# Optimization experiments

Hardware: AMD Instinct MI355X
Metric: run time of the kernel (lower is better)

The kernel has to match this reference:

```python
import jax, jax.numpy as jnp
import numpy as np

BETA = 0.1
MARGIN = 0.1
LOSS_WEIGHT = 1.0
K = 4          # num_negative_samples_per_positive
EPS = 1e-6
C, D, P = 100000, 256, 65536


def _energy(p, c):
    """Euclidean entailment-cone energy: relu(apex_angle(p,c) - aperture(p))."""
    diff = c - p
    num = jnp.sum(c * c, -1) - jnp.sum(p * p, -1) - jnp.sum(diff * diff, -1)
    norm_p = jnp.linalg.norm(p, axis=-1)
    denom = 2.0 * norm_p * jnp.linalg.norm(diff, axis=-1) + EPS
    cosang = jnp.clip(num / denom, -1.0 + EPS, 1.0 - EPS)
    ang = jnp.arccos(cosang)
    aperture = jnp.arcsin(jnp.clip(BETA / (norm_p + EPS), 0.0, 1.0 - EPS))
    return jax.nn.relu(ang - aperture)


def setup_inputs() -> dict:
    key = jax.random.key(0)
    k1, k2, k3 = jax.random.split(key, 3)
    prototypes = jax.random.normal(k1, (C, D), dtype=jnp.float32)
    pairs = jax.random.randint(k2, (P, 2), 0, C, dtype=jnp.int32)
    neg_c = jax.random.randint(k3, (P * K,), 0, C, dtype=jnp.int32)
    return {"prototypes": prototypes, "pairs": pairs, "neg_c": neg_c}


def reference(prototypes, pairs, neg_c):
    # positive pairs: (parent, child) gathers
    p_pos = prototypes[pairs[:, 0]]                    # [P, D]
    c_pos = prototypes[pairs[:, 1]]                    # [P, D]
    avg_pos = _energy(p_pos, c_pos).mean()

    # negatives: each positive parent repeated K times vs sampled neg children
    neg_p_idx = jnp.repeat(pairs[:, 0], K)             # [P*K]
    p_neg = prototypes[neg_p_idx]                      # [P*K, D]
    c_neg = prototypes[neg_c]                          # [P*K, D]
    avg_neg = jax.nn.relu(MARGIN - _energy(p_neg, c_neg)).mean()

    return (avg_pos + avg_neg) * 0.5 * LOSS_WEIGHT
```

## Files before the change

kernel.cpp:

```cpp
#include <hip/hip_runtime.h>

#define BETA   0.1f
#define MARGIN 0.1f
#define EPSF   1e-6f
#define KNEG   4

typedef float f2_t __attribute__((ext_vector_type(2)));

__device__ __forceinline__ float gsum16(float v) {
    #pragma unroll
    for (int off = 8; off >= 1; off >>= 1) v += __shfl_xor(v, off, 64);
    return v;
}
__device__ __forceinline__ float wave_sum(float v) {
    #pragma unroll
    for (int off = 32; off >= 1; off >>= 1) v += __shfl_xor(v, off, 64);
    return v;
}
__device__ __forceinline__ float dot4(float4 a, float4 b) {
    return a.x*b.x + a.y*b.y + a.z*b.z + a.w*b.w;
}
__device__ __forceinline__ void unpack4(unsigned int u, float* f) {
    f2_t a = __builtin_amdgcn_cvt_pk_f32_fp8(u, false);
    f[0] = a.x; f[1] = a.y;
    a = __builtin_amdgcn_cvt_pk_f32_fp8(u, true);
    f[2] = a.x; f[3] = a.y;
}

__global__ __launch_bounds__(256) void cvt_fp8(
    const float* __restrict__ in, unsigned int* __restrict__ out, int n4)
{
    int i = blockIdx.x * 256 + threadIdx.x;
    const int stride = gridDim.x * 256;
    const float4* in4 = (const float4*)in;
    for (; i < n4; i += stride) {
        float4 v = in4[i];
        unsigned int p = __builtin_amdgcn_cvt_pk_fp8_f32(v.x, v.y, 0u, false);
        p = __builtin_amdgcn_cvt_pk_fp8_f32(v.z, v.w, p, true);
        out[i] = p;
    }
}

__global__ __launch_bounds__(256) void cone_main_fp8(
    const uint4* __restrict__ tab,
    const int*   __restrict__ pairs,
    const int*   __restrict__ negc,
    float*       __restrict__ part,
    int P)
{
    const int lane = threadIdx.x & 63;
    const int wid  = threadIdx.x >> 6;
    const int sub  = lane >> 4;
    const int sl   = lane & 15;
    const int pair = (blockIdx.x * 4 + wid) * 4 + sub;

    float pos_e = 0.f, neg_e = 0.f;
    if (pair < P) {
        const int pi = pairs[2 * pair];
        int idx[5];
        idx[0] = pairs[2 * pair + 1];
        #pragma unroll
        for (int k = 0; k < KNEG; ++k) idx[1 + k] = negc[4 * pair + k];

        uint4 pu = tab[(size_t)pi * 16 + sl];
        uint4 cu[5];
        #pragma unroll
        for (int j = 0; j < 5; ++j) cu[j] = tab[(size_t)idx[j] * 16 + sl];

        float pf[16];
        unpack4(pu.x, pf + 0);  unpack4(pu.y, pf + 4);
        unpack4(pu.z, pf + 8);  unpack4(pu.w, pf + 12);
        float pp = 0.f;
        #pragma unroll
        for (int d = 0; d < 16; ++d) pp += pf[d] * pf[d];
        float p2     = gsum16(pp);
        float norm_p = sqrtf(p2);
        float apert  = asinf(fminf(fmaxf(BETA / (norm_p + EPSF), 0.f), 1.f - EPSF));

        #pragma unroll
        for (int j = 0; j < 5; ++j) {
            float cf[16];
            unpack4(cu[j].x, cf + 0);  unpack4(cu[j].y, cf + 4);
            unpack4(cu[j].z, cf + 8);  unpack4(cu[j].w, cf + 12);
            float cc = 0.f, dd = 0.f;
            #pragma unroll
            for (int d = 0; d < 16; ++d) {
                cc += cf[d] * cf[d];
                float t = cf[d] - pf[d];
                dd += t * t;
            }
            float c2 = gsum16(cc);
            float d2 = gsum16(dd);
            float num    = c2 - p2 - d2;
            float den    = 2.f * norm_p * sqrtf(d2) + EPSF;
            float cosang = fminf(fmaxf(num / den, -1.f + EPSF), 1.f - EPSF);
            float e      = fmaxf(acosf(cosang) - apert, 0.f);
            if (j == 0) pos_e = e;
            else        neg_e += fmaxf(MARGIN - e, 0.f);
        }
    }

    __shared__ float sp[16], sn[16];
    if (sl == 0) { sp[wid * 4 + sub] = pos_e; sn[wid * 4 + sub] = neg_e; }
    __syncthreads();
    if (threadIdx.x == 0) {
        float ps = 0.f, ns = 0.f;
        #pragma unroll
        for (int i = 0; i < 16; ++i) { ps += sp[i]; ns += sn[i]; }
        part[2 * blockIdx.x]     = ps;
        part[2 * blockIdx.x + 1] = ns;
    }
}

__global__ __launch_bounds__(256) void cone_main_f32(
    const float* __restrict__ proto,
    const int*   __restrict__ pairs,
    const int*   __restrict__ negc,
    float*       __restrict__ part,
    int P)
{
    const int lane = threadIdx.x & 63;
    const int wid  = threadIdx.x >> 6;
    const int sub  = lane >> 4;
    const int sl   = lane & 15;
    const int pair = (blockIdx.x * 4 + wid) * 4 + sub;

    float pos_e = 0.f, neg_e = 0.f;
    if (pair < P) {
        const int pi = pairs[2 * pair];
        int idx[5];
        idx[0] = pairs[2 * pair + 1];
        #pragma unroll
        for (int k = 0; k < KNEG; ++k) idx[1 + k] = negc[4 * pair + k];

        const float4* prow = (const float4*)(proto + (size_t)pi * 256);
        float4 pv[4];
        #pragma unroll
        for (int r = 0; r < 4; ++r) pv[r] = prow[sl + 16 * r];

        float pp = 0.f;
        #pragma unroll
        for (int r = 0; r < 4; ++r) pp += dot4(pv[r], pv[r]);
        float p2     = gsum16(pp);
        float norm_p = sqrtf(p2);
        float apert  = asinf(fminf(fmaxf(BETA / (norm_p + EPSF), 0.f), 1.f - EPSF));

        #pragma unroll
        for (int j = 0; j < 5; ++j) {
            const float4* crow = (const float4*)(proto + (size_t)idx[j] * 256);
            float cc = 0.f, dd = 0.f;
            #pragma unroll
            for (int r = 0; r < 4; ++r) {
                float4 c = crow[sl + 16 * r], p = pv[r];
                cc += dot4(c, c);
                float dx = c.x - p.x, dy = c.y - p.y, dz = c.z - p.z, dw = c.w - p.w;
                dd += dx*dx + dy*dy + dz*dz + dw*dw;
            }
            float c2 = gsum16(cc);
            float d2 = gsum16(dd);
            float num    = c2 - p2 - d2;
            float den    = 2.f * norm_p * sqrtf(d2) + EPSF;
            float cosang = fminf(fmaxf(num / den, -1.f + EPSF), 1.f - EPSF);
            float e      = fmaxf(acosf(cosang) - apert, 0.f);
            if (j == 0) pos_e = e;
            else        neg_e += fmaxf(MARGIN - e, 0.f);
        }
    }

    __shared__ float sp[16], sn[16];
    if (sl == 0) { sp[wid * 4 + sub] = pos_e; sn[wid * 4 + sub] = neg_e; }
    __syncthreads();
    if (threadIdx.x == 0) {
        float ps = 0.f, ns = 0.f;
        #pragma unroll
        for (int i = 0; i < 16; ++i) { ps += sp[i]; ns += sn[i]; }
        part[2 * blockIdx.x]     = ps;
        part[2 * blockIdx.x + 1] = ns;
    }
}

__global__ __launch_bounds__(1024) void cone_final(
    const float* __restrict__ part, float* __restrict__ out, int nblocks, int P)
{
    float ps = 0.f, ns = 0.f;
    for (int i = threadIdx.x; i < nblocks; i += 1024) {
        ps += part[2 * i];
        ns += part[2 * i + 1];
    }
    ps = wave_sum(ps);
    ns = wave_sum(ns);
    const int lane = threadIdx.x & 63, wid = threadIdx.x >> 6;
    __shared__ float sp[16], sn[16];
    if (lane == 0) { sp[wid] = ps; sn[wid] = ns; }
    __syncthreads();
    if (threadIdx.x == 0) {
        float tp = 0.f, tn = 0.f;
        #pragma unroll
        for (int i = 0; i < 16; ++i) { tp += sp[i]; tn += sn[i]; }
        float fP = (float)P;
        out[0] = (tp / fP + tn / (fP * (float)KNEG)) * 0.5f;
    }
}

extern "C" void kernel_launch(void* const* d_in, const int* in_sizes, int n_in,
                              void* d_out, int out_size, void* d_ws, size_t ws_size,
                              hipStream_t stream) {
    const float* proto = (const float*)d_in[0];
    const int*   pairs = (const int*)d_in[1];
    const int*   negc  = (const int*)d_in[2];
    const int P = in_sizes[1] / 2;
    const int nblocks = (P + 15) / 16;

    const size_t tab_bytes = (size_t)in_sizes[0];
    const size_t need = tab_bytes + (size_t)nblocks * 2 * sizeof(float);

    if (ws_size >= need) {
        unsigned int* tab  = (unsigned int*)d_ws;
        float*        part = (float*)((char*)d_ws + tab_bytes);
        const int n4 = in_sizes[0] / 4;
        cvt_fp8<<<8192, 256, 0, stream>>>(proto, tab, n4);
        cone_main_fp8<<<nblocks, 256, 0, stream>>>((const uint4*)tab, pairs, negc, part, P);
        cone_final<<<1, 1024, 0, stream>>>(part, (float*)d_out, nblocks, P);
    } else {
        float* part = (float*)d_ws;
        cone_main_f32<<<nblocks, 256, 0, stream>>>(proto, pairs, negc, part, P);
        cone_final<<<1, 1024, 0, stream>>>(part, (float*)d_out, nblocks, P);
    }
}
```

Measured before the change: 177.2 us.

## Precompute per-row fp32 norms and apertures during fp8 conversion; use dot-product identity

The conversion kernel now processes one row per 16 lanes, packs it to fp8 and also stores each row's squared norm (in fp32) and cone aperture. The main kernel fetches these per-row scalars with one lane-distributed gather plus shuffles. It rewrites the energy using the single dot product p·c (d2 = c2 + p2 - 2dot, num = 2(dot - p2)), which removes two of three reductions and the per-pair asin. This trades a slightly heavier conversion pass and extra workspace for less ALU and shuffle work in the main kernel. Norms come from fp32 rather than fp8 values, and the identity can cancel numerically, which the code guards by clamping d2 at zero.

```diff
diff --git a/kernel.cpp b/kernel.cpp
--- a/kernel.cpp
+++ b/kernel.cpp
@@ -20,29 +20,41 @@
 __device__ __forceinline__ float dot4(float4 a, float4 b) {
     return a.x*b.x + a.y*b.y + a.z*b.z + a.w*b.w;
 }
-__device__ __forceinline__ void unpack4(unsigned int u, float* f) {
+__device__ __forceinline__ unsigned packf4(float4 v) {
+    unsigned p = __builtin_amdgcn_cvt_pk_fp8_f32(v.x, v.y, 0u, false);
+    return __builtin_amdgcn_cvt_pk_fp8_f32(v.z, v.w, p, true);
+}
+__device__ __forceinline__ void unpack4(unsigned u, float* f) {
     f2_t a = __builtin_amdgcn_cvt_pk_f32_fp8(u, false);
     f[0] = a.x; f[1] = a.y;
     a = __builtin_amdgcn_cvt_pk_f32_fp8(u, true);
     f[2] = a.x; f[3] = a.y;
 }
 
-__global__ __launch_bounds__(256) void cvt_fp8(
-    const float* __restrict__ in, unsigned int* __restrict__ out, int n4)
-{
-    int i = blockIdx.x * 256 + threadIdx.x;
-    const int stride = gridDim.x * 256;
-    const float4* in4 = (const float4*)in;
-    for (; i < n4; i += stride) {
-        float4 v = in4[i];
-        unsigned int p = __builtin_amdgcn_cvt_pk_fp8_f32(v.x, v.y, 0u, false);
-        p = __builtin_amdgcn_cvt_pk_fp8_f32(v.z, v.w, p, true);
-        out[i] = p;
+__global__ __launch_bounds__(256) void cvt_fp8_norm(
+    const float* __restrict__ in, uint4* __restrict__ tab,
+    float* __restrict__ norm2, float* __restrict__ apert, int C)
+{
+    const int sl  = threadIdx.x & 15;
+    const int row = (blockIdx.x * 256 + threadIdx.x) >> 4;
+    if (row >= C) return;
+    const float4* src = (const float4*)(in + (size_t)row * 256);
+    float4 v0 = src[sl], v1 = src[sl + 16], v2 = src[sl + 32], v3 = src[sl + 48];
+    uint4 u;
+    u.x = packf4(v0); u.y = packf4(v1); u.z = packf4(v2); u.w = packf4(v3);
+    tab[(size_t)row * 16 + sl] = u;
+    float ss = gsum16(dot4(v0,v0) + dot4(v1,v1) + dot4(v2,v2) + dot4(v3,v3));
+    if (sl == 0) {
+        norm2[row] = ss;
+        float np = sqrtf(ss);
+        apert[row] = asinf(fminf(fmaxf(BETA / (np + EPSF), 0.f), 1.f - EPSF));
     }
 }
 
 __global__ __launch_bounds__(256) void cone_main_fp8(
     const uint4* __restrict__ tab,
+    const float* __restrict__ norm2,
+    const float* __restrict__ apert,
     const int*   __restrict__ pairs,
     const int*   __restrict__ negc,
     float*       __restrict__ part,
@@ -67,34 +79,33 @@
         #pragma unroll
         for (int j = 0; j < 5; ++j) cu[j] = tab[(size_t)idx[j] * 16 + sl];
 
+        int tidx = (sl >= 2 && sl < 7) ? idx[sl - 2] : pi;
+        const float* tbl = (sl == 1) ? apert : norm2;
+        float sv = tbl[tidx];
+        const int base = sub * 16;
+        const float p2 = __shfl(sv, base + 0, 64);
+        const float ap = __shfl(sv, base + 1, 64);
+        const float np = sqrtf(p2);
+
         float pf[16];
         unpack4(pu.x, pf + 0);  unpack4(pu.y, pf + 4);
         unpack4(pu.z, pf + 8);  unpack4(pu.w, pf + 12);
-        float pp = 0.f;
-        #pragma unroll
-        for (int d = 0; d < 16; ++d) pp += pf[d] * pf[d];
-        float p2     = gsum16(pp);
-        float norm_p = sqrtf(p2);
-        float apert  = asinf(fminf(fmaxf(BETA / (norm_p + EPSF), 0.f), 1.f - EPSF));
 
         #pragma unroll
         for (int j = 0; j < 5; ++j) {
             float cf[16];
             unpack4(cu[j].x, cf + 0);  unpack4(cu[j].y, cf + 4);
             unpack4(cu[j].z, cf + 8);  unpack4(cu[j].w, cf + 12);
-            float cc = 0.f, dd = 0.f;
+            float acc = 0.f;
             #pragma unroll
-            for (int d = 0; d < 16; ++d) {
-                cc += cf[d] * cf[d];
-                float t = cf[d] - pf[d];
-                dd += t * t;
-            }
-            float c2 = gsum16(cc);
-            float d2 = gsum16(dd);
-            float num    = c2 - p2 - d2;
-            float den    = 2.f * norm_p * sqrtf(d2) + EPSF;
-            float cosang = fminf(fmaxf(num / den, -1.f + EPSF), 1.f - EPSF);
-            float e      = fmaxf(acosf(cosang) - apert, 0.f);
+            for (int d = 0; d < 16; ++d) acc += cf[d] * pf[d];
+            float dot = gsum16(acc);
+            float c2  = __shfl(sv, base + 2 + j, 64);
+            float num = 2.f * (dot - p2);
+            float d2  = fmaxf(c2 + p2 - 2.f * dot, 0.f);
+            float den = 2.f * np * sqrtf(d2) + EPSF;
+            float ca  = fminf(fmaxf(num / den, -1.f + EPSF), 1.f - EPSF);
+            float e   = fmaxf(acosf(ca) - ap, 0.f);
             if (j == 0) pos_e = e;
             else        neg_e += fmaxf(MARGIN - e, 0.f);
         }
@@ -209,17 +220,20 @@
     const int*   pairs = (const int*)d_in[1];
     const int*   negc  = (const int*)d_in[2];
     const int P = in_sizes[1] / 2;
+    const int C = in_sizes[0] / 256;
     const int nblocks = (P + 15) / 16;
 
     const size_t tab_bytes = (size_t)in_sizes[0];
-    const size_t need = tab_bytes + (size_t)nblocks * 2 * sizeof(float);
+    const size_t need = tab_bytes + (size_t)C * 2 * sizeof(float)
+                      + (size_t)nblocks * 2 * sizeof(float);
 
     if (ws_size >= need) {
-        unsigned int* tab  = (unsigned int*)d_ws;
-        float*        part = (float*)((char*)d_ws + tab_bytes);
-        const int n4 = in_sizes[0] / 4;
-        cvt_fp8<<<8192, 256, 0, stream>>>(proto, tab, n4);
-        cone_main_fp8<<<nblocks, 256, 0, stream>>>((const uint4*)tab, pairs, negc, part, P);
+        uint4* tab   = (uint4*)d_ws;
+        float* norm2 = (float*)((char*)d_ws + tab_bytes);
+        float* apert = norm2 + C;
+        float* part  = apert + C;
+        cvt_fp8_norm<<<(C + 15) / 16, 256, 0, stream>>>(proto, tab, norm2, apert, C);
+        cone_main_fp8<<<nblocks, 256, 0, stream>>>(tab, norm2, apert, pairs, negc, part, P);
         cone_final<<<1, 1024, 0, stream>>>(part, (float*)d_out, nblocks, P);
     } else {
         float* part = (float*)d_ws;
```

New measurement: 174.7 us. No clear change (-1.4%).
